# Kernel optimization log

Hardware: AMD Instinct MI355X
Metric: run time of the kernel (lower is better)

The kernel has to match this reference:

```python
import jax, jax.numpy as jnp
import numpy as np
from jax import lax

TEMP = 65.0
CLIP_DIST = 0.01
EPS = 1e-6  # torch PairwiseDistance eps (added to the difference) and log eps
NTOKEN, NINP, NHID = 32000, 1024, 1024
SEQ_LEN, BSZ, NSAMPLES = 128, 64, 10


def setup_inputs() -> dict:
    key = jax.random.key(0)
    ks = jax.random.split(key, 7)
    data = jax.random.randint(ks[0], (SEQ_LEN, BSZ), 0, NTOKEN)
    samples = jax.random.randint(ks[1], (NSAMPLES, SEQ_LEN * BSZ), 0, NTOKEN)
    # encoder init_weights: uniform(-0.1, 0.1); RNN weights small to avoid tanh saturation
    emb_W = jax.random.uniform(ks[2], (NTOKEN, NINP), minval=-0.1, maxval=0.1, dtype=jnp.float32)
    W_ih = jax.random.normal(ks[3], (NHID, NINP), dtype=jnp.float32) * 0.03
    b_ih = jax.random.normal(ks[4], (NHID,), dtype=jnp.float32) * 0.01
    W_hh = jax.random.normal(ks[5], (NHID, NHID), dtype=jnp.float32) * 0.03
    b_hh = jax.random.normal(ks[6], (NHID,), dtype=jnp.float32) * 0.01
    return {"data": data, "samples": samples, "emb_W": emb_W,
            "W_ih": W_ih, "b_ih": b_ih, "W_hh": W_hh, "b_hh": b_hh}


def _sq_pdist(x, y):
    # torch PairwiseDistance(p=2).pow(2): ||x - y + eps||^2 (no sqrt needed)
    d = x - y + EPS
    return jnp.sum(d * d, axis=-1)


def reference(data, samples, emb_W, W_ih, b_ih, W_hh, b_hh):
    seq_len, bsz = data.shape
    nhid = W_hh.shape[0]
    emb = emb_W[data]                                  # [S, B, ninp]
    h0 = jnp.zeros((bsz, nhid), dtype=emb_W.dtype)

    def step(h, e):
        h_new = jnp.tanh(e @ W_ih.T + b_ih + h @ W_hh.T + b_hh)
        return h_new, h_new

    _, outs = lax.scan(step, h0, emb)                  # [S, B, H]
    raw = jnp.concatenate([h0[None], outs], axis=0)    # [S+1, B, H]

    # positive term: temp * ||h_t - h_{t+1}||^2, summed, averaged over seq_len
    pos = TEMP * _sq_pdist(raw[:-1], raw[1:])          # [S, B]
    loss = pos.sum() / seq_len

    prev = raw[:-1].reshape(seq_len * bsz, nhid)       # [S*B, H]
    samples_emb = emb_W[samples]                       # [ns, S*B, ninp]
    samples_W = samples_emb @ W_ih.T + b_ih            # [ns, S*B, H]
    hiddens_U = prev @ W_hh.T + b_hh                   # [S*B, H]

    out = jnp.tanh(samples_W + hiddens_U[None])        # [ns, S*B, H]
    dist = _sq_pdist(prev[None], out)                  # [ns, S*B]
    dist = jnp.clip(dist, 0.0, CLIP_DIST)
    n = seq_len * bsz
    sum_of_exp = jnp.sum(jnp.exp(-dist), axis=0) / n   # [S*B]
    loss = loss + jnp.log(sum_of_exp + EPS).sum()
    return loss
```

## Files before the change

kernel.cpp:

```cpp
#include <hip/hip_runtime.h>
#include <hip/hip_bf16.h>
#include <cmath>

typedef __bf16 bf16;
typedef __attribute__((ext_vector_type(8))) __bf16 bf16x8;
typedef __attribute__((ext_vector_type(4))) __bf16 bf16x4;
typedef __attribute__((ext_vector_type(4))) float f32x4;
typedef unsigned long long ull;

#define TEMPC 65.0f
#define EPSC 1e-6f

#define GLD_LDS16(gptr, lptr)                                                             \
    __builtin_amdgcn_global_load_lds(                                                     \
        (const __attribute__((address_space(1))) unsigned int*)(gptr),                    \
        (__attribute__((address_space(3))) unsigned int*)(lptr), 16, 0, 0)

__global__ void conv_kernel(const float* __restrict__ s, bf16* __restrict__ d, int n)
{
    int i = (blockIdx.x * blockDim.x + threadIdx.x) * 4;
    const int stride = gridDim.x * blockDim.x * 4;
    for (; i < n; i += stride) {
        const float4 v = *(const float4*)(s + i);
        bf16x4 o;
        o[0] = (bf16)v.x; o[1] = (bf16)v.y; o[2] = (bf16)v.z; o[3] = (bf16)v.w;
        *(bf16x4*)(d + i) = o;
    }
}

__global__ __launch_bounds__(256)
void gemm0_kernel(const int* __restrict__ idx, const bf16* __restrict__ emb,
                  const bf16* __restrict__ Wmat, const float* __restrict__ bih,
                  bf16* __restrict__ XWout)
{
    __shared__ __align__(16) bf16 As[2 * 128 * 32];
    __shared__ __align__(16) bf16 Bs[2 * 128 * 32];

    const int tid = threadIdx.x;
    const int l  = tid & 63;
    const int w  = tid >> 6;
    const int wr = w >> 1, wc = w & 1;
    const int wg = (blockIdx.x & 7) * 64 + (blockIdx.x >> 3);
    const int mbase = (wg >> 3) * 128;
    const int nbase = (wg & 7) * 128;

    const int r0 = w * 32 + (l >> 2);
    const int csw = ((l & 3) ^ ((l >> 3) & 3)) * 16;
    const char* Asrc0 = (const char*)emb + (size_t)idx[mbase + r0] * 2048 + csw;
    const char* Asrc1 = (const char*)emb + (size_t)idx[mbase + r0 + 16] * 2048 + csw;
    const char* Bsrc0 = (const char*)Wmat + (size_t)(nbase + r0) * 2048 + csw;
    const char* Bsrc1 = (const char*)Wmat + (size_t)(nbase + r0 + 16) * 2048 + csw;

    const int frow  = l & 15;
    const int koffE = (((l >> 4) ^ ((frow >> 1) & 3)) * 8);
    const bf16* Ard = As + (wr * 64 + frow) * 32 + koffE;
    const bf16* Brd = Bs + (wc * 64 + frow) * 32 + koffE;

    auto stage = [&](int buf, int kb) {
        bf16* As_ = As + buf * 4096 + w * 1024;
        bf16* Bs_ = Bs + buf * 4096 + w * 1024;
        GLD_LDS16(Asrc0 + kb, As_);
        GLD_LDS16(Asrc1 + kb, As_ + 512);
        GLD_LDS16(Bsrc0 + kb, Bs_);
        GLD_LDS16(Bsrc1 + kb, Bs_ + 512);
    };

    stage(0, 0);
    stage(1, 64);

    f32x4 acc[4][4] = {};
    for (int k = 0; k < 32; ++k) {
        if (k == 31) asm volatile("s_waitcnt vmcnt(0)" ::: "memory");
        else         asm volatile("s_waitcnt vmcnt(4)" ::: "memory");
        __builtin_amdgcn_s_barrier();
        const bf16* Ab = Ard + (k & 1) * 4096;
        const bf16* Bb = Brd + (k & 1) * 4096;
        bf16x8 af[4], bfr[4];
        #pragma unroll
        for (int mt = 0; mt < 4; ++mt) af[mt]  = *(const bf16x8*)(Ab + mt * 16 * 32);
        #pragma unroll
        for (int nt = 0; nt < 4; ++nt) bfr[nt] = *(const bf16x8*)(Bb + nt * 16 * 32);
        #pragma unroll
        for (int mt = 0; mt < 4; ++mt)
            #pragma unroll
            for (int nt = 0; nt < 4; ++nt)
                acc[mt][nt] = __builtin_amdgcn_mfma_f32_16x16x32_bf16(af[mt], bfr[nt], acc[mt][nt], 0, 0, 0);
        asm volatile("s_waitcnt lgkmcnt(0)" ::: "memory");
        __builtin_amdgcn_s_barrier();
        if (k + 2 < 32) stage(k & 1, (k + 2) * 64);
    }

    #pragma unroll
    for (int mt = 0; mt < 4; ++mt)
        #pragma unroll
        for (int nt = 0; nt < 4; ++nt) {
            const int colg = nbase + wc * 64 + nt * 16 + frow;
            const float bi = bih[colg];
            #pragma unroll
            for (int r = 0; r < 4; ++r) {
                const int rowg = mbase + wr * 64 + mt * 16 + (l >> 4) * 4 + r;
                XWout[(size_t)rowg * 1024 + colg] = (bf16)(acc[mt][nt][r] + bi);
            }
        }
}

__global__ __launch_bounds__(256, 1)
void fused_kernel(const bf16* __restrict__ emb, const bf16* __restrict__ Wih,
                  const float* __restrict__ bih, bf16* __restrict__ P,
                  bf16* __restrict__ raw, const bf16* __restrict__ Whh,
                  const bf16* __restrict__ XWb, const float* __restrict__ bhh,
                  bf16* __restrict__ Ust, int* __restrict__ cnt)
{
    __shared__ __align__(16) char pool[147584];
    const int tid = threadIdx.x;
    const int l   = tid & 63;
    const int w   = tid >> 6;
    const int id  = blockIdx.x;

    if (id < 128) {
        bf16* Wlds = (bf16*)pool;
        char* Hlds = pool + 131072;
        const int group  = id & 7;
        const int slot   = id >> 3;
        const int jbase  = slot * 64;
        const int frow   = l & 15;
        const int kchunk = l >> 4;
        const int jglob  = jbase + w * 16 + frow;
        const int rr     = frow & 7;

        {
            const int jloc = l >> 2;
            const int csw  = ((l & 3) ^ ((l >> 3) & 3)) * 16;
            const char* gsrc = (const char*)Whh + (size_t)(jbase + w * 16 + jloc) * 2048 + csw;
            for (int kk = 0; kk < 32; ++kk)
                GLD_LDS16(gsrc + kk * 64, Wlds + (kk * 4 + w) * 512);
            asm volatile("s_waitcnt vmcnt(0)" ::: "memory");
            __syncthreads();
        }
        const float bh = bhh[jglob];

        const int ksw   = kchunk ^ ((frow >> 1) & 3);
        const bf16* wrd = Wlds + w * 512 + frow * 32 + ksw * 8;
        const char* hrd = Hlds + rr * 2064 + kchunk * 16;

        for (int t = 0; t < 128; ++t) {
            if (t > 0) {
                if (tid < 4)
                    while (__hip_atomic_load(&cnt[((t * 8 + group) * 4 + tid) * 32],
                                             __ATOMIC_RELAXED, __HIP_MEMORY_SCOPE_AGENT) < 4)
                        __builtin_amdgcn_s_sleep(1);
                __syncthreads();
            }
            const ull* hsrc8 = (const ull*)(raw + (size_t)t * 65536 + group * 8192);
            ull hv[8];
            #pragma unroll
            for (int i = 0; i < 8; ++i)
                hv[i] = __hip_atomic_load(hsrc8 + tid + i * 256,
                                          __ATOMIC_RELAXED, __HIP_MEMORY_SCOPE_AGENT);
            float xw[4];
            #pragma unroll
            for (int r = 0; r < 4; ++r) {
                const int bc = (kchunk * 4 + r) & 7;
                xw[r] = (float)XWb[(size_t)(t * 64 + group * 8 + bc) * 1024 + jglob];
            }
            #pragma unroll
            for (int i = 0; i < 8; ++i)
                *(ull*)(Hlds + i * 2064 + tid * 8) = hv[i];
            __syncthreads();

            f32x4 acc0 = {0.f,0.f,0.f,0.f}, acc1 = {0.f,0.f,0.f,0.f};
            #pragma unroll
            for (int kk = 0; kk < 32; kk += 2) {
                bf16x8 a0 = *(const bf16x8*)(hrd + kk * 64);
                bf16x8 a1 = *(const bf16x8*)(hrd + kk * 64 + 64);
                acc0 = __builtin_amdgcn_mfma_f32_16x16x32_bf16(a0, *(const bf16x8*)(wrd + kk * 2048),       acc0, 0, 0, 0);
                acc1 = __builtin_amdgcn_mfma_f32_16x16x32_bf16(a1, *(const bf16x8*)(wrd + (kk + 1) * 2048), acc1, 0, 0, 0);
            }

            bf16* rawN = raw + (size_t)(t + 1) * 65536;
            if (l < 32) {
                #pragma unroll
                for (int r = 0; r < 4; ++r) {
                    const int b = (l >> 4) * 4 + r;
                    const float V = acc0[r] + acc1[r] + bh;
                    const float h = tanhf(xw[r] + V);
                    const size_t row = (size_t)(t * 64 + group * 8 + b);
                    Ust[row * 1024 + jglob] = (bf16)V;
                    const bf16 hb = (bf16)h;
                    unsigned short hs = __builtin_bit_cast(unsigned short, hb);
                    unsigned short hn = (unsigned short)__shfl_down((int)hs, 1, 64);
                    if ((frow & 1) == 0) {
                        unsigned int pack = (unsigned int)hs | ((unsigned int)hn << 16);
                        unsigned int* dst = (unsigned int*)(rawN + (size_t)(group * 8 + b) * 1024 + jglob);
                        __hip_atomic_store(dst, pack, __ATOMIC_RELAXED, __HIP_MEMORY_SCOPE_AGENT);
                    }
                }
            }
            if (t < 127) {
                __syncthreads();
                if (tid == 0)
                    __hip_atomic_fetch_add(&cnt[(((t + 1) * 8 + group) * 4 + (slot & 3)) * 32], 1,
                                           __ATOMIC_RELAXED, __HIP_MEMORY_SCOPE_AGENT);
            }
        }
    } else {
        bf16* As = (bf16*)pool;
        bf16* Bs = (bf16*)(pool + 16384);
        const int q  = id - 128;
        const int wg = (q & 7) * 250 + (q >> 3);
        const int mbase = (wg >> 3) * 128;
        const int nbase = (wg & 7) * 128;
        const int wr = w >> 1, wc = w & 1;

        const int r0 = w * 32 + (l >> 2);
        const int csw = ((l & 3) ^ ((l >> 3) & 3)) * 16;
        const char* Asrc0 = (const char*)emb + (size_t)(mbase + r0) * 2048 + csw;
        const char* Asrc1 = (const char*)emb + (size_t)(mbase + r0 + 16) * 2048 + csw;
        const char* Bsrc0 = (const char*)Wih + (size_t)(nbase + r0) * 2048 + csw;
        const char* Bsrc1 = (const char*)Wih + (size_t)(nbase + r0 + 16) * 2048 + csw;

        const int frow  = l & 15;
        const int koffE = (((l >> 4) ^ ((frow >> 1) & 3)) * 8);
        const bf16* Ard = As + (wr * 64 + frow) * 32 + koffE;
        const bf16* Brd = Bs + (wc * 64 + frow) * 32 + koffE;

        auto stage = [&](int buf, int kb) {
            bf16* As_ = As + buf * 4096 + w * 1024;
            bf16* Bs_ = Bs + buf * 4096 + w * 1024;
            GLD_LDS16(Asrc0 + kb, As_);
            GLD_LDS16(Asrc1 + kb, As_ + 512);
            GLD_LDS16(Bsrc0 + kb, Bs_);
            GLD_LDS16(Bsrc1 + kb, Bs_ + 512);
        };

        stage(0, 0);
        stage(1, 64);

        f32x4 acc[4][4] = {};
        for (int k = 0; k < 32; ++k) {
            if (k == 31) asm volatile("s_waitcnt vmcnt(0)" ::: "memory");
            else         asm volatile("s_waitcnt vmcnt(4)" ::: "memory");
            __builtin_amdgcn_s_barrier();
            const bf16* Ab = Ard + (k & 1) * 4096;
            const bf16* Bb = Brd + (k & 1) * 4096;
            bf16x8 af[4], bfr[4];
            #pragma unroll
            for (int mt = 0; mt < 4; ++mt) af[mt]  = *(const bf16x8*)(Ab + mt * 16 * 32);
            #pragma unroll
            for (int nt = 0; nt < 4; ++nt) bfr[nt] = *(const bf16x8*)(Bb + nt * 16 * 32);
            #pragma unroll
            for (int mt = 0; mt < 4; ++mt)
                #pragma unroll
                for (int nt = 0; nt < 4; ++nt)
                    acc[mt][nt] = __builtin_amdgcn_mfma_f32_16x16x32_bf16(af[mt], bfr[nt], acc[mt][nt], 0, 0, 0);
            asm volatile("s_waitcnt lgkmcnt(0)" ::: "memory");
            __builtin_amdgcn_s_barrier();
            if (k + 2 < 32) stage(k & 1, (k + 2) * 64);
        }

        #pragma unroll
        for (int mt = 0; mt < 4; ++mt)
            #pragma unroll
            for (int nt = 0; nt < 4; ++nt) {
                const int colg = nbase + wc * 64 + nt * 16 + frow;
                const float bi = bih[colg];
                #pragma unroll
                for (int r = 0; r < 4; ++r) {
                    const int rowg = mbase + wr * 64 + mt * 16 + (l >> 4) * 4 + r;
                    P[(size_t)rowg * 1024 + colg] = (bf16)(acc[mt][nt][r] + bi);
                }
            }
    }
}

__global__ void pos_kernel(const bf16* __restrict__ raw, float* __restrict__ lacc)
{
    float s = 0.f;
    const int NV = (128 * 64 * 1024) / 8;
    for (int i = blockIdx.x * blockDim.x + threadIdx.x; i < NV; i += gridDim.x * blockDim.x) {
        bf16x8 a = *(const bf16x8*)(raw + (size_t)i * 8);
        bf16x8 b = *(const bf16x8*)(raw + (size_t)i * 8 + 65536);
        #pragma unroll
        for (int j = 0; j < 8; ++j) {
            const float d = (float)a[j] - (float)b[j] + EPSC;
            s += d * d;
        }
    }
    #pragma unroll
    for (int off = 32; off > 0; off >>= 1) s += __shfl_down(s, off, 64);
    if ((threadIdx.x & 63) == 0) atomicAdd(lacc, s * (TEMPC / 128.f));
}

__global__ __launch_bounds__(256)
void neg_kernel(const int* __restrict__ samples, const bf16* __restrict__ P,
                const bf16* __restrict__ Ust, const bf16* __restrict__ raw,
                float* __restrict__ lacc)
{
    const int l = threadIdx.x & 63;
    const int r = blockIdx.x * 4 + (threadIdx.x >> 6);
    const bf16* u  = Ust + (size_t)r * 1024;
    const bf16* pv = raw + (size_t)r * 1024;

    float uf[16], vf[16];
    {
        bf16x8 u0 = *(const bf16x8*)(u + l * 8);
        bf16x8 u1 = *(const bf16x8*)(u + 512 + l * 8);
        bf16x8 v0 = *(const bf16x8*)(pv + l * 8);
        bf16x8 v1 = *(const bf16x8*)(pv + 512 + l * 8);
        #pragma unroll
        for (int i = 0; i < 8; ++i) {
            uf[i] = (float)u0[i]; uf[8 + i] = (float)u1[i];
            vf[i] = (float)v0[i]; vf[8 + i] = (float)v1[i];
        }
    }

    float se = 0.f;
    #pragma unroll
    for (int s = 0; s < 10; ++s) {
        const int tok = samples[s * 8192 + r];
        const bf16* pr = P + (size_t)tok * 1024;
        bf16x8 p0 = *(const bf16x8*)(pr + l * 8);
        bf16x8 p1 = *(const bf16x8*)(pr + 512 + l * 8);
        float d2 = 0.f;
        #pragma unroll
        for (int i = 0; i < 8; ++i) {
            const float o0 = tanhf((float)p0[i] + uf[i]);
            const float d0 = vf[i] - o0 + EPSC;
            d2 += d0 * d0;
            const float o1 = tanhf((float)p1[i] + uf[8 + i]);
            const float d1 = vf[8 + i] - o1 + EPSC;
            d2 += d1 * d1;
        }
        #pragma unroll
        for (int off = 1; off < 64; off <<= 1)
            d2 += __shfl_xor(d2, off, 64);
        se += expf(-fminf(d2, 0.01f));
    }
    if (l == 0) atomicAdd(lacc, logf(se * (1.f / 8192.f) + EPSC));
}

__global__ void fin_kernel(const float* __restrict__ lacc, float* __restrict__ out)
{
    if (threadIdx.x == 0) out[0] = lacc[0];
}

extern "C" void kernel_launch(void* const* d_in, const int* in_sizes, int n_in,
                              void* d_out, int out_size, void* d_ws, size_t ws_size,
                              hipStream_t stream)
{
    const int*   data    = (const int*)d_in[0];
    const int*   samples = (const int*)d_in[1];
    const float* emb     = (const float*)d_in[2];
    const float* Wih     = (const float*)d_in[3];
    const float* bih     = (const float*)d_in[4];
    const float* Whh     = (const float*)d_in[5];
    const float* bhh     = (const float*)d_in[6];

    char* ws = (char*)d_ws;
    size_t off = 0;
    auto alloc = [&](size_t bytes) { void* p = ws + off; off += (bytes + 255) & ~(size_t)255; return p; };
    bf16*  emb_b = (bf16*)alloc((size_t)32000 * 1024 * 2);
    bf16*  Wih_b = (bf16*)alloc((size_t)1024 * 1024 * 2);
    bf16*  Whh_b = (bf16*)alloc((size_t)1024 * 1024 * 2);
    bf16*  P     = (bf16*)alloc((size_t)32000 * 1024 * 2);
    bf16*  XWb   = (bf16*)alloc((size_t)8192 * 1024 * 2);
    bf16*  Ust   = (bf16*)alloc((size_t)8192 * 1024 * 2);
    bf16*  raw   = (bf16*)alloc((size_t)129 * 64 * 1024 * 2);
    float* lacc  = (float*)alloc(256);
    int*   cnt   = (int*)alloc(524288);

    hipMemsetAsync(raw, 0, 64 * 1024 * 2, stream);
    hipMemsetAsync(lacc, 0, 256, stream);
    hipMemsetAsync(cnt,  0, 524288, stream);

    conv_kernel<<<2048, 256, 0, stream>>>(emb, emb_b, 32000 * 1024);
    conv_kernel<<<512, 256, 0, stream>>>(Wih, Wih_b, 1024 * 1024);
    conv_kernel<<<512, 256, 0, stream>>>(Whh, Whh_b, 1024 * 1024);

    gemm0_kernel<<<512, 256, 0, stream>>>(data, emb_b, Wih_b, bih, XWb);

    fused_kernel<<<2128, 256, 0, stream>>>(emb_b, Wih_b, bih, P,
                                           raw, Whh_b, XWb, bhh, Ust, cnt);

    pos_kernel<<<512, 256, 0, stream>>>(raw, lacc);

    neg_kernel<<<2048, 256, 0, stream>>>(samples, P, Ust, raw, lacc);

    fin_kernel<<<1, 64, 0, stream>>>(lacc, (float*)d_out);
}
```

Before: 665.3 us.

## Fuse input-projection GEMM and positive loss into recurrent kernel with sentinel polling

Merges the three fp32-to-bf16 conversion kernels into one launch. It also moves the data-embedding input-projection GEMM into the fused persistent kernel as extra blocks, which publish results with atomic stores. The recurrent blocks poll for a 0xFFFFFFFF sentinel in a buffer pre-filled by memset, so the recurrence can start before the whole projection is done. The positive-pair distance term is now accumulated inside the recurrence, which removes the separate pos_kernel pass over raw. The risks are spin-waiting if the projection blocks are scheduled late, a bf16 value that happens to match the sentinel bit pattern, and an extra 16 MB memset.

Result: faster. 577.2 us (-13.2%).

```diff
diff --git a/kernel.cpp b/kernel.cpp
--- a/kernel.cpp
+++ b/kernel.cpp
@@ -16,100 +16,36 @@
         (const __attribute__((address_space(1))) unsigned int*)(gptr),                    \
         (__attribute__((address_space(3))) unsigned int*)(lptr), 16, 0, 0)
 
-__global__ void conv_kernel(const float* __restrict__ s, bf16* __restrict__ d, int n)
-{
-    int i = (blockIdx.x * blockDim.x + threadIdx.x) * 4;
+__global__ void conv3_kernel(const float* __restrict__ e, bf16* __restrict__ eb,
+                             const float* __restrict__ a, bf16* __restrict__ ab,
+                             const float* __restrict__ b, bf16* __restrict__ bb)
+{
+    const int base   = (blockIdx.x * blockDim.x + threadIdx.x) * 4;
     const int stride = gridDim.x * blockDim.x * 4;
-    for (; i < n; i += stride) {
-        const float4 v = *(const float4*)(s + i);
-        bf16x4 o;
-        o[0] = (bf16)v.x; o[1] = (bf16)v.y; o[2] = (bf16)v.z; o[3] = (bf16)v.w;
-        *(bf16x4*)(d + i) = o;
-    }
-}
-
-__global__ __launch_bounds__(256)
-void gemm0_kernel(const int* __restrict__ idx, const bf16* __restrict__ emb,
-                  const bf16* __restrict__ Wmat, const float* __restrict__ bih,
-                  bf16* __restrict__ XWout)
-{
-    __shared__ __align__(16) bf16 As[2 * 128 * 32];
-    __shared__ __align__(16) bf16 Bs[2 * 128 * 32];
-
-    const int tid = threadIdx.x;
-    const int l  = tid & 63;
-    const int w  = tid >> 6;
-    const int wr = w >> 1, wc = w & 1;
-    const int wg = (blockIdx.x & 7) * 64 + (blockIdx.x >> 3);
-    const int mbase = (wg >> 3) * 128;
-    const int nbase = (wg & 7) * 128;
-
-    const int r0 = w * 32 + (l >> 2);
-    const int csw = ((l & 3) ^ ((l >> 3) & 3)) * 16;
-    const char* Asrc0 = (const char*)emb + (size_t)idx[mbase + r0] * 2048 + csw;
-    const char* Asrc1 = (const char*)emb + (size_t)idx[mbase + r0 + 16] * 2048 + csw;
-    const char* Bsrc0 = (const char*)Wmat + (size_t)(nbase + r0) * 2048 + csw;
-    const char* Bsrc1 = (const char*)Wmat + (size_t)(nbase + r0 + 16) * 2048 + csw;
-
-    const int frow  = l & 15;
-    const int koffE = (((l >> 4) ^ ((frow >> 1) & 3)) * 8);
-    const bf16* Ard = As + (wr * 64 + frow) * 32 + koffE;
-    const bf16* Brd = Bs + (wc * 64 + frow) * 32 + koffE;
-
-    auto stage = [&](int buf, int kb) {
-        bf16* As_ = As + buf * 4096 + w * 1024;
-        bf16* Bs_ = Bs + buf * 4096 + w * 1024;
-        GLD_LDS16(Asrc0 + kb, As_);
-        GLD_LDS16(Asrc1 + kb, As_ + 512);
-        GLD_LDS16(Bsrc0 + kb, Bs_);
-        GLD_LDS16(Bsrc1 + kb, Bs_ + 512);
-    };
-
-    stage(0, 0);
-    stage(1, 64);
-
-    f32x4 acc[4][4] = {};
-    for (int k = 0; k < 32; ++k) {
-        if (k == 31) asm volatile("s_waitcnt vmcnt(0)" ::: "memory");
-        else         asm volatile("s_waitcnt vmcnt(4)" ::: "memory");
-        __builtin_amdgcn_s_barrier();
-        const bf16* Ab = Ard + (k & 1) * 4096;
-        const bf16* Bb = Brd + (k & 1) * 4096;
-        bf16x8 af[4], bfr[4];
-        #pragma unroll
-        for (int mt = 0; mt < 4; ++mt) af[mt]  = *(const bf16x8*)(Ab + mt * 16 * 32);
-        #pragma unroll
-        for (int nt = 0; nt < 4; ++nt) bfr[nt] = *(const bf16x8*)(Bb + nt * 16 * 32);
-        #pragma unroll
-        for (int mt = 0; mt < 4; ++mt)
-            #pragma unroll
-            for (int nt = 0; nt < 4; ++nt)
-                acc[mt][nt] = __builtin_amdgcn_mfma_f32_16x16x32_bf16(af[mt], bfr[nt], acc[mt][nt], 0, 0, 0);
-        asm volatile("s_waitcnt lgkmcnt(0)" ::: "memory");
-        __builtin_amdgcn_s_barrier();
-        if (k + 2 < 32) stage(k & 1, (k + 2) * 64);
-    }
-
-    #pragma unroll
-    for (int mt = 0; mt < 4; ++mt)
-        #pragma unroll
-        for (int nt = 0; nt < 4; ++nt) {
-            const int colg = nbase + wc * 64 + nt * 16 + frow;
-            const float bi = bih[colg];
-            #pragma unroll
-            for (int r = 0; r < 4; ++r) {
-                const int rowg = mbase + wr * 64 + mt * 16 + (l >> 4) * 4 + r;
-                XWout[(size_t)rowg * 1024 + colg] = (bf16)(acc[mt][nt][r] + bi);
-            }
-        }
+    for (int i = base; i < 32000 * 1024; i += stride) {
+        const float4 v = *(const float4*)(e + i);
+        bf16x4 o; o[0]=(bf16)v.x; o[1]=(bf16)v.y; o[2]=(bf16)v.z; o[3]=(bf16)v.w;
+        *(bf16x4*)(eb + i) = o;
+    }
+    for (int i = base; i < 1024 * 1024; i += stride) {
+        const float4 v = *(const float4*)(a + i);
+        bf16x4 o; o[0]=(bf16)v.x; o[1]=(bf16)v.y; o[2]=(bf16)v.z; o[3]=(bf16)v.w;
+        *(bf16x4*)(ab + i) = o;
+    }
+    for (int i = base; i < 1024 * 1024; i += stride) {
+        const float4 v = *(const float4*)(b + i);
+        bf16x4 o; o[0]=(bf16)v.x; o[1]=(bf16)v.y; o[2]=(bf16)v.z; o[3]=(bf16)v.w;
+        *(bf16x4*)(bb + i) = o;
+    }
 }
 
 __global__ __launch_bounds__(256, 1)
-void fused_kernel(const bf16* __restrict__ emb, const bf16* __restrict__ Wih,
-                  const float* __restrict__ bih, bf16* __restrict__ P,
-                  bf16* __restrict__ raw, const bf16* __restrict__ Whh,
-                  const bf16* __restrict__ XWb, const float* __restrict__ bhh,
-                  bf16* __restrict__ Ust, int* __restrict__ cnt)
+void fused_kernel(const int* __restrict__ data, const bf16* __restrict__ emb,
+                  const bf16* __restrict__ Wih, const float* __restrict__ bih,
+                  bf16* __restrict__ P, bf16* __restrict__ raw,
+                  const bf16* __restrict__ Whh, bf16* __restrict__ XWb,
+                  const float* __restrict__ bhh, bf16* __restrict__ Ust,
+                  int* __restrict__ cnt, float* __restrict__ lacc)
 {
     __shared__ __align__(16) char pool[147584];
     const int tid = threadIdx.x;
@@ -142,6 +78,8 @@
         const int ksw   = kchunk ^ ((frow >> 1) & 3);
         const bf16* wrd = Wlds + w * 512 + frow * 32 + ksw * 8;
         const char* hrd = Hlds + rr * 2064 + kchunk * 16;
+        const int jpair = jglob & ~1;
+        float posacc = 0.f;
 
         for (int t = 0; t < 128; ++t) {
             if (t > 0) {
@@ -157,11 +95,13 @@
             for (int i = 0; i < 8; ++i)
                 hv[i] = __hip_atomic_load(hsrc8 + tid + i * 256,
                                           __ATOMIC_RELAXED, __HIP_MEMORY_SCOPE_AGENT);
-            float xw[4];
+            unsigned int xww[4];
             #pragma unroll
             for (int r = 0; r < 4; ++r) {
                 const int bc = (kchunk * 4 + r) & 7;
-                xw[r] = (float)XWb[(size_t)(t * 64 + group * 8 + bc) * 1024 + jglob];
+                const size_t row = (size_t)(t * 64 + group * 8 + bc);
+                xww[r] = __hip_atomic_load((const unsigned int*)(XWb + row * 1024 + jpair),
+                                           __ATOMIC_RELAXED, __HIP_MEMORY_SCOPE_AGENT);
             }
             #pragma unroll
             for (int i = 0; i < 8; ++i)
@@ -177,16 +117,37 @@
                 acc1 = __builtin_amdgcn_mfma_f32_16x16x32_bf16(a1, *(const bf16x8*)(wrd + (kk + 1) * 2048), acc1, 0, 0, 0);
             }
 
+            for (;;) {
+                bool bad = false;
+                #pragma unroll
+                for (int r = 0; r < 4; ++r) bad |= (xww[r] == 0xFFFFFFFFu);
+                if (!bad) break;
+                #pragma unroll
+                for (int r = 0; r < 4; ++r)
+                    if (xww[r] == 0xFFFFFFFFu) {
+                        const int bc = (kchunk * 4 + r) & 7;
+                        const size_t row = (size_t)(t * 64 + group * 8 + bc);
+                        xww[r] = __hip_atomic_load((const unsigned int*)(XWb + row * 1024 + jpair),
+                                                   __ATOMIC_RELAXED, __HIP_MEMORY_SCOPE_AGENT);
+                    }
+            }
+
             bf16* rawN = raw + (size_t)(t + 1) * 65536;
             if (l < 32) {
                 #pragma unroll
                 for (int r = 0; r < 4; ++r) {
                     const int b = (l >> 4) * 4 + r;
+                    const unsigned short x16 = (jglob & 1) ? (unsigned short)(xww[r] >> 16)
+                                                           : (unsigned short)(xww[r] & 0xFFFF);
+                    const float xwv = __builtin_bit_cast(float, (unsigned int)x16 << 16);
                     const float V = acc0[r] + acc1[r] + bh;
-                    const float h = tanhf(xw[r] + V);
+                    const float h = tanhf(xwv + V);
                     const size_t row = (size_t)(t * 64 + group * 8 + b);
                     Ust[row * 1024 + jglob] = (bf16)V;
                     const bf16 hb = (bf16)h;
+                    const float ht = (float)*(const bf16*)(Hlds + b * 2064 + jglob * 2);
+                    const float pd = ht - (float)hb + EPSC;
+                    posacc += pd * pd;
                     unsigned short hs = __builtin_bit_cast(unsigned short, hb);
                     unsigned short hn = (unsigned short)__shfl_down((int)hs, 1, 64);
                     if ((frow & 1) == 0) {
@@ -203,19 +164,33 @@
                                            __ATOMIC_RELAXED, __HIP_MEMORY_SCOPE_AGENT);
             }
         }
+        #pragma unroll
+        for (int off2 = 32; off2 > 0; off2 >>= 1) posacc += __shfl_down(posacc, off2, 64);
+        if (l == 0) atomicAdd(lacc, posacc * (TEMPC / 128.f));
     } else {
         bf16* As = (bf16*)pool;
         bf16* Bs = (bf16*)(pool + 16384);
-        const int q  = id - 128;
-        const int wg = (q & 7) * 250 + (q >> 3);
-        const int mbase = (wg >> 3) * 128;
-        const int nbase = (wg & 7) * 128;
         const int wr = w >> 1, wc = w & 1;
-
+        const bool isXW = (id < 640);
+
+        int mbase, nbase;
+        const char *Asrc0, *Asrc1;
         const int r0 = w * 32 + (l >> 2);
         const int csw = ((l & 3) ^ ((l >> 3) & 3)) * 16;
-        const char* Asrc0 = (const char*)emb + (size_t)(mbase + r0) * 2048 + csw;
-        const char* Asrc1 = (const char*)emb + (size_t)(mbase + r0 + 16) * 2048 + csw;
+        if (isXW) {
+            const int q = id - 128;
+            mbase = (q >> 3) * 128;
+            nbase = (q & 7) * 128;
+            Asrc0 = (const char*)emb + (size_t)data[mbase + r0] * 2048 + csw;
+            Asrc1 = (const char*)emb + (size_t)data[mbase + r0 + 16] * 2048 + csw;
+        } else {
+            const int q  = id - 640;
+            const int wg = (q & 7) * 250 + (q >> 3);
+            mbase = (wg >> 3) * 128;
+            nbase = (wg & 7) * 128;
+            Asrc0 = (const char*)emb + (size_t)(mbase + r0) * 2048 + csw;
+            Asrc1 = (const char*)emb + (size_t)(mbase + r0 + 16) * 2048 + csw;
+        }
         const char* Bsrc0 = (const char*)Wih + (size_t)(nbase + r0) * 2048 + csw;
         const char* Bsrc1 = (const char*)Wih + (size_t)(nbase + r0 + 16) * 2048 + csw;
 
@@ -258,37 +233,41 @@
             if (k + 2 < 32) stage(k & 1, (k + 2) * 64);
         }
 
-        #pragma unroll
-        for (int mt = 0; mt < 4; ++mt)
-            #pragma unroll
-            for (int nt = 0; nt < 4; ++nt) {
-                const int colg = nbase + wc * 64 + nt * 16 + frow;
-                const float bi = bih[colg];
-                #pragma unroll
-                for (int r = 0; r < 4; ++r) {
-                    const int rowg = mbase + wr * 64 + mt * 16 + (l >> 4) * 4 + r;
-                    P[(size_t)rowg * 1024 + colg] = (bf16)(acc[mt][nt][r] + bi);
+        if (isXW) {
+            #pragma unroll
+            for (int mt = 0; mt < 4; ++mt)
+                #pragma unroll
+                for (int nt = 0; nt < 4; ++nt) {
+                    const int colg = nbase + wc * 64 + nt * 16 + frow;
+                    const float bi = bih[colg];
+                    #pragma unroll
+                    for (int r = 0; r < 4; ++r) {
+                        const int rowg = mbase + wr * 64 + mt * 16 + (l >> 4) * 4 + r;
+                        const bf16 vb = (bf16)(acc[mt][nt][r] + bi);
+                        unsigned short vs = __builtin_bit_cast(unsigned short, vb);
+                        unsigned short vn = (unsigned short)__shfl_down((int)vs, 1, 64);
+                        if ((frow & 1) == 0) {
+                            unsigned int pack = (unsigned int)vs | ((unsigned int)vn << 16);
+                            __hip_atomic_store((unsigned int*)(XWb + (size_t)rowg * 1024 + colg),
+                                               pack, __ATOMIC_RELAXED, __HIP_MEMORY_SCOPE_AGENT);
+                        }
+                    }
                 }
-            }
-    }
-}
-
-__global__ void pos_kernel(const bf16* __restrict__ raw, float* __restrict__ lacc)
-{
-    float s = 0.f;
-    const int NV = (128 * 64 * 1024) / 8;
-    for (int i = blockIdx.x * blockDim.x + threadIdx.x; i < NV; i += gridDim.x * blockDim.x) {
-        bf16x8 a = *(const bf16x8*)(raw + (size_t)i * 8);
-        bf16x8 b = *(const bf16x8*)(raw + (size_t)i * 8 + 65536);
-        #pragma unroll
-        for (int j = 0; j < 8; ++j) {
-            const float d = (float)a[j] - (float)b[j] + EPSC;
-            s += d * d;
-        }
-    }
-    #pragma unroll
-    for (int off = 32; off > 0; off >>= 1) s += __shfl_down(s, off, 64);
-    if ((threadIdx.x & 63) == 0) atomicAdd(lacc, s * (TEMPC / 128.f));
+        } else {
+            #pragma unroll
+            for (int mt = 0; mt < 4; ++mt)
+                #pragma unroll
+                for (int nt = 0; nt < 4; ++nt) {
+                    const int colg = nbase + wc * 64 + nt * 16 + frow;
+                    const float bi = bih[colg];
+                    #pragma unroll
+                    for (int r = 0; r < 4; ++r) {
+                        const int rowg = mbase + wr * 64 + mt * 16 + (l >> 4) * 4 + r;
+                        P[(size_t)rowg * 1024 + colg] = (bf16)(acc[mt][nt][r] + bi);
+                    }
+                }
+        }
+    }
 }
 
 __global__ __launch_bounds__(256)
@@ -370,19 +349,14 @@
     int*   cnt   = (int*)alloc(524288);
 
     hipMemsetAsync(raw, 0, 64 * 1024 * 2, stream);
+    hipMemsetAsync(XWb, 0xFF, (size_t)8192 * 1024 * 2, stream);
     hipMemsetAsync(lacc, 0, 256, stream);
     hipMemsetAsync(cnt,  0, 524288, stream);
 
-    conv_kernel<<<2048, 256, 0, stream>>>(emb, emb_b, 32000 * 1024);
-    conv_kernel<<<512, 256, 0, stream>>>(Wih, Wih_b, 1024 * 1024);
-    conv_kernel<<<512, 256, 0, stream>>>(Whh, Whh_b, 1024 * 1024);
-
-    gemm0_kernel<<<512, 256, 0, stream>>>(data, emb_b, Wih_b, bih, XWb);
-
-    fused_kernel<<<2128, 256, 0, stream>>>(emb_b, Wih_b, bih, P,
-                                           raw, Whh_b, XWb, bhh, Ust, cnt);
-
-    pos_kernel<<<512, 256, 0, stream>>>(raw, lacc);
+    conv3_kernel<<<2048, 256, 0, stream>>>(emb, emb_b, Wih, Wih_b, Whh, Whh_b);
+
+    fused_kernel<<<2640, 256, 0, stream>>>(data, emb_b, Wih_b, bih, P,
+                                           raw, Whh_b, XWb, bhh, Ust, cnt, lacc);
 
     neg_kernel<<<2048, 256, 0, stream>>>(samples, P, Ust, raw, lacc);
 
```
